# Optimization experiments

Hardware: AMD Instinct MI355X
Metric: run time of the kernel (lower is better)

The kernel has to match this reference:

```python
import jax, jax.numpy as jnp
import numpy as np
from jax import lax


def setup_inputs() -> dict:
    key = jax.random.key(0)
    k1, k2 = jax.random.split(key)
    L, B, D = 1024, 16, 1024
    x = jax.random.normal(k1, (L, B, D), dtype=jnp.float32)
    # weight maps n_in -> n_out*k with k=3 (n_in == n_out); small scale for stability
    weight = jax.random.normal(k2, (D, 3 * D), dtype=jnp.float32) * 0.05
    bias = jnp.zeros((2 * D,), dtype=jnp.float32)
    c0 = jnp.zeros((B, D), dtype=jnp.float32)
    return {"x": x, "weight": weight, "bias": bias, "c0": c0}


def reference(x, weight, bias, c0):
    # SRUCell forward, k == 3 (n_in == n_out), unidirectional, tanh activation,
    # no dropout masks (mask_h == NULL -> mask = 1).
    L, B, D = x.shape
    u = (x.reshape(L * B, D) @ weight).reshape(L, B, D, 3)
    b1 = bias[:D]
    b2 = bias[D:]
    u0 = u[..., 0]                                   # [L, B, D]
    g1 = jax.nn.sigmoid(u[..., 1] + b1)              # forget gate
    g2 = jax.nn.sigmoid(u[..., 2] + b2)              # reset/highway gate

    def step(c, inp):
        u0_t, g1_t, g2_t, x_t = inp
        c_new = (c - u0_t) * g1_t + u0_t             # c = c'*g1 + u0*(1-g1)
        h_t = (jnp.tanh(c_new) - x_t) * g2_t + x_t   # h = act(c)*g2 + x*(1-g2)
        return c_new, h_t

    c_last, h = lax.scan(step, c0, (u0, g1, g2, x))
    return h, c_last
```

## Files before the change

### kernel.cpp

```cpp
#include <hip/hip_runtime.h>

#define L_DIM 1024
#define B_DIM 16
#define D_DIM 1024
#define K_DIM 1024
#define N_DIM 3072
#define M_DIM (L_DIM * B_DIM)
#define CHAINS 16384
#define CHUNK 64
#define NCHUNK 16

typedef float f32x4 __attribute__((ext_vector_type(4)));
typedef __bf16 bf16x8 __attribute__((ext_vector_type(8)));
typedef unsigned short u16;
typedef unsigned int u32;

__device__ __forceinline__ u16 f2bf(float f) {
  u32 u = __float_as_uint(f);
  u = u + 0x7FFFu + ((u >> 16) & 1u);
  return (u16)(u >> 16);
}
__device__ __forceinline__ float bf2f(u16 v) {
  return __uint_as_float(((u32)v) << 16);
}
__device__ __forceinline__ float fexp(float v) {
  return __builtin_amdgcn_exp2f(v * 1.4426950408889634f);
}
__device__ __forceinline__ float sigm(float z) {
  return __builtin_amdgcn_rcpf(1.0f + fexp(-z));
}
__device__ __forceinline__ float ftanh(float v) {
  return 1.0f - 2.0f * __builtin_amdgcn_rcpf(1.0f + fexp(2.0f * v));
}

__global__ __launch_bounds__(256) void cvt_x_kernel(const float4* __restrict__ in,
                                                    ushort4* __restrict__ out, int n4) {
  int i = blockIdx.x * 256 + threadIdx.x;
  if (i < n4) {
    float4 v = in[i];
    ushort4 o;
    o.x = f2bf(v.x); o.y = f2bf(v.y); o.z = f2bf(v.z); o.w = f2bf(v.w);
    out[i] = o;
  }
}

__global__ __launch_bounds__(256) void cvt_w_kernel(const float* __restrict__ W,
                                                    u16* __restrict__ Wt) {
  __shared__ float tile[64][65];
  int c0 = blockIdx.x * 64;
  int r0 = blockIdx.y * 64;
  int tx = threadIdx.x & 63;
  int ty = threadIdx.x >> 6;
#pragma unroll
  for (int i = 0; i < 16; ++i) {
    int row = i * 4 + ty;
    tile[row][tx] = W[(size_t)(r0 + row) * N_DIM + c0 + tx];
  }
  __syncthreads();
#pragma unroll
  for (int i = 0; i < 16; ++i) {
    int crow = i * 4 + ty;
    int c = c0 + crow;
    int nprime = (c % 3) * D_DIM + (c / 3);
    Wt[(size_t)nprime * K_DIM + r0 + tx] = f2bf(tile[tx][crow]);
  }
}

__global__ __launch_bounds__(256) void gemm_kernel(const u16* __restrict__ A,
                                                   const u16* __restrict__ Bt,
                                                   u16* __restrict__ U) {
  __shared__ u16 lA[128 * 32];
  __shared__ u16 lB[128 * 32];
  const int tid = threadIdx.x;
  const int wave = tid >> 6;
  const int lane = tid & 63;
  const int wm = wave >> 1, wn = wave & 1;
  const int quad = lane >> 4, l16 = lane & 15;
  const int m0 = blockIdx.y * 128;
  const int n0 = blockIdx.x * 128;

  f32x4 acc[4][4] = {};

  const u16* gA = A + (size_t)(m0 + (tid >> 2)) * K_DIM + (tid & 3) * 8;
  const u16* gB = Bt + (size_t)(n0 + (tid >> 2)) * K_DIM + (tid & 3) * 8;
  u16* sA0 = lA + wave * 512;
  u16* sA1 = lA + 2048 + wave * 512;
  u16* sB0 = lB + wave * 512;
  u16* sB1 = lB + 2048 + wave * 512;

  const u16* rA = lA + (wm * 64 + l16) * 32 + quad * 8;
  const u16* rB = lB + (wn * 64 + l16) * 32 + quad * 8;

  for (int k0 = 0; k0 < K_DIM; k0 += 32) {
    __syncthreads();
    __builtin_amdgcn_global_load_lds((const __attribute__((address_space(1))) void*)(gA + k0),
                                     (__attribute__((address_space(3))) void*)sA0, 16, 0, 0);
    __builtin_amdgcn_global_load_lds((const __attribute__((address_space(1))) void*)(gA + (size_t)64 * K_DIM + k0),
                                     (__attribute__((address_space(3))) void*)sA1, 16, 0, 0);
    __builtin_amdgcn_global_load_lds((const __attribute__((address_space(1))) void*)(gB + k0),
                                     (__attribute__((address_space(3))) void*)sB0, 16, 0, 0);
    __builtin_amdgcn_global_load_lds((const __attribute__((address_space(1))) void*)(gB + (size_t)64 * K_DIM + k0),
                                     (__attribute__((address_space(3))) void*)sB1, 16, 0, 0);
    __syncthreads();

    bf16x8 af[4], bfr[4];
#pragma unroll
    for (int mt = 0; mt < 4; ++mt) af[mt] = *(const bf16x8*)(rA + mt * 16 * 32);
#pragma unroll
    for (int nt = 0; nt < 4; ++nt) bfr[nt] = *(const bf16x8*)(rB + nt * 16 * 32);
#pragma unroll
    for (int mt = 0; mt < 4; ++mt)
#pragma unroll
      for (int nt = 0; nt < 4; ++nt)
        acc[mt][nt] = __builtin_amdgcn_mfma_f32_16x16x32_bf16(af[mt], bfr[nt], acc[mt][nt], 0, 0, 0);
  }

#pragma unroll
  for (int mt = 0; mt < 4; ++mt) {
#pragma unroll
    for (int nt = 0; nt < 4; ++nt) {
      int col = n0 + wn * 64 + nt * 16 + l16;
      int rbase = m0 + wm * 64 + mt * 16 + quad * 4;
#pragma unroll
      for (int r = 0; r < 4; ++r) {
        U[(size_t)(rbase + r) * N_DIM + col] = f2bf(acc[mt][nt][r]);
      }
    }
  }
}


__global__ __launch_bounds__(256) void sru_phase1(const u16* __restrict__ U,
                                                  const float* __restrict__ bias,
                                                  float* __restrict__ Aarr,
                                                  float* __restrict__ Barr) {
  int tid = blockIdx.x * 256 + threadIdx.x;
  int chain = tid & (CHAINS - 1);
  int j = tid >> 14;
  int d = chain & (D_DIM - 1);
  int b = chain >> 10;
  float bb1 = bias[d];
  const u16* p = U + (size_t)(j * CHUNK * B_DIM + b) * N_DIM + d;
  float A = 1.0f, Bv = 0.0f;
#pragma unroll 4
  for (int s = 0; s < CHUNK; ++s) {
    float u0 = bf2f(p[0]);
    float g1 = sigm(bf2f(p[D_DIM]) + bb1);
    Bv = (Bv - u0) * g1 + u0;
    A *= g1;
    p += (size_t)B_DIM * N_DIM;
  }
  Aarr[tid] = A;
  Barr[tid] = Bv;
}

__global__ __launch_bounds__(256) void sru_phase2(const float* __restrict__ Aarr,
                                                  const float* __restrict__ Barr,
                                                  const float* __restrict__ c0,
                                                  float* __restrict__ Cin,
                                                  float* __restrict__ clast) {
  int chain = blockIdx.x * 256 + threadIdx.x;
  float As[NCHUNK], Bs[NCHUNK];
#pragma unroll
  for (int j = 0; j < NCHUNK; ++j) {
    As[j] = Aarr[j * CHAINS + chain];
    Bs[j] = Barr[j * CHAINS + chain];
  }
  float c = c0[chain];
#pragma unroll
  for (int j = 0; j < NCHUNK; ++j) {
    Cin[j * CHAINS + chain] = c;
    c = As[j] * c + Bs[j];
  }
  clast[chain] = c;
}

__global__ __launch_bounds__(256) void sru_phase3(const u16* __restrict__ U,
                                                  const float* __restrict__ x,
                                                  const float* __restrict__ bias,
                                                  const float* __restrict__ Cin,
                                                  float* __restrict__ h) {
  int tid = blockIdx.x * 256 + threadIdx.x;
  int chain = tid & (CHAINS - 1);
  int j = tid >> 14;
  int d = chain & (D_DIM - 1);
  int b = chain >> 10;
  float bb1 = bias[d];
  float bb2 = bias[D_DIM + d];
  float c = Cin[tid];
  size_t m0 = (size_t)(j * CHUNK * B_DIM + b);
  const u16* p = U + m0 * N_DIM + d;
  const float* xp = x + m0 * D_DIM + d;
  float* hp = h + m0 * D_DIM + d;
#pragma unroll 4
  for (int s = 0; s < CHUNK; ++s) {
    float u0 = bf2f(p[0]);
    float g1 = sigm(bf2f(p[D_DIM]) + bb1);
    float g2 = sigm(bf2f(p[2 * D_DIM]) + bb2);
    c = (c - u0) * g1 + u0;
    float xv = *xp;
    *hp = (ftanh(c) - xv) * g2 + xv;
    p += (size_t)B_DIM * N_DIM;
    xp += B_DIM * D_DIM;
    hp += B_DIM * D_DIM;
  }
}

extern "C" void kernel_launch(void* const* d_in, const int* in_sizes, int n_in,
                              void* d_out, int out_size, void* d_ws, size_t ws_size,
                              hipStream_t stream) {
  const float* x = (const float*)d_in[0];
  const float* W = (const float*)d_in[1];
  const float* bias = (const float*)d_in[2];
  const float* c0 = (const float*)d_in[3];
  float* out = (float*)d_out;

  char* ws = (char*)d_ws;
  u16* xb = (u16*)ws;
  u16* wt = (u16*)(ws + 33554432);
  u16* U = (u16*)(ws + 33554432 + 6291456);
  float* Aarr = (float*)ws;
  float* Barr = (float*)(ws + 1048576);
  float* Cin  = (float*)(ws + 2097152);

  cvt_x_kernel<<<16384, 256, 0, stream>>>((const float4*)x, (ushort4*)xb, M_DIM * K_DIM / 4);
  cvt_w_kernel<<<dim3(48, 16), 256, 0, stream>>>(W, wt);
  gemm_kernel<<<dim3(N_DIM / 128, M_DIM / 128), 256, 0, stream>>>(xb, wt, U);
  sru_phase1<<<CHAINS * NCHUNK / 256, 256, 0, stream>>>(U, bias, Aarr, Barr);
  sru_phase2<<<CHAINS / 256, 256, 0, stream>>>(Aarr, Barr, c0, Cin, out + (size_t)M_DIM * D_DIM);
  sru_phase3<<<CHAINS * NCHUNK / 256, 256, 0, stream>>>(U, x, bias, Cin, out);
}
```

Before: 299.9 us.

## Stage GEMM output through LDS and vectorize scan phases eight channels per thread

The GEMM epilogue now writes bf16 results into a padded LDS tile and then stores 16-byte rows to global memory, replacing scattered 2-byte stores. The scan phases 1 and 3 now process eight adjacent channels per thread with 16-byte loads of U, x and h. The chunk count is doubled (32 chunks of 32 steps) so enough threads remain for parallelism, and the Aarr/Barr/Cin workspace offsets grow to match. Phase 2 now reads Aarr/Barr inside the loop instead of preloading them into register arrays, and the added chunks lengthen its serial chain.

```diff
diff --git a/kernel.cpp b/kernel.cpp
--- a/kernel.cpp
+++ b/kernel.cpp
@@ -7,13 +7,14 @@
 #define N_DIM 3072
 #define M_DIM (L_DIM * B_DIM)
 #define CHAINS 16384
-#define CHUNK 64
-#define NCHUNK 16
+#define CHUNK 32
+#define NCHUNK 32
 
 typedef float f32x4 __attribute__((ext_vector_type(4)));
 typedef __bf16 bf16x8 __attribute__((ext_vector_type(8)));
 typedef unsigned short u16;
 typedef unsigned int u32;
+typedef u16 u16x8 __attribute__((ext_vector_type(8)));
 
 __device__ __forceinline__ u16 f2bf(float f) {
   u32 u = __float_as_uint(f);
@@ -69,8 +70,9 @@
 __global__ __launch_bounds__(256) void gemm_kernel(const u16* __restrict__ A,
                                                    const u16* __restrict__ Bt,
                                                    u16* __restrict__ U) {
-  __shared__ u16 lA[128 * 32];
-  __shared__ u16 lB[128 * 32];
+  __shared__ __align__(16) char smem[128 * 132 * 2];
+  u16* lA = (u16*)smem;
+  u16* lB = (u16*)(smem + 8192);
   const int tid = threadIdx.x;
   const int wave = tid >> 6;
   const int lane = tid & 63;
@@ -115,17 +117,30 @@
         acc[mt][nt] = __builtin_amdgcn_mfma_f32_16x16x32_bf16(af[mt], bfr[nt], acc[mt][nt], 0, 0, 0);
   }
 
+  __syncthreads();
+  u16* lC = (u16*)smem;
 #pragma unroll
   for (int mt = 0; mt < 4; ++mt) {
 #pragma unroll
     for (int nt = 0; nt < 4; ++nt) {
-      int col = n0 + wn * 64 + nt * 16 + l16;
-      int rbase = m0 + wm * 64 + mt * 16 + quad * 4;
-#pragma unroll
-      for (int r = 0; r < 4; ++r) {
-        U[(size_t)(rbase + r) * N_DIM + col] = f2bf(acc[mt][nt][r]);
-      }
+      int row = wm * 64 + mt * 16 + quad * 4;
+      int col = wn * 64 + nt * 16 + l16;
+#pragma unroll
+      for (int r = 0; r < 4; ++r)
+        lC[(row + r) * 132 + col] = f2bf(acc[mt][nt][r]);
     }
+  }
+  __syncthreads();
+  int g = tid & 15;
+  int r0w = tid >> 4;
+#pragma unroll
+  for (int it = 0; it < 8; ++it) {
+    int row = r0w + it * 16;
+    const u16* src = lC + row * 132 + g * 8;
+    uint2 lo = *(const uint2*)src;
+    uint2 hi = *(const uint2*)(src + 4);
+    uint4 v = make_uint4(lo.x, lo.y, hi.x, hi.y);
+    *(uint4*)(U + (size_t)(m0 + row) * N_DIM + n0 + g * 8) = v;
   }
 }
 
@@ -135,23 +150,37 @@
                                                   float* __restrict__ Aarr,
                                                   float* __restrict__ Barr) {
   int tid = blockIdx.x * 256 + threadIdx.x;
-  int chain = tid & (CHAINS - 1);
-  int j = tid >> 14;
-  int d = chain & (D_DIM - 1);
-  int b = chain >> 10;
-  float bb1 = bias[d];
-  const u16* p = U + (size_t)(j * CHUNK * B_DIM + b) * N_DIM + d;
-  float A = 1.0f, Bv = 0.0f;
+  int j = tid >> 11;
+  int b = (tid >> 7) & 15;
+  int dg = tid & 127;
+  int d0 = dg * 8;
+  int chain0 = b * D_DIM + d0;
+  float bb1[8];
+#pragma unroll
+  for (int i = 0; i < 8; ++i) bb1[i] = bias[d0 + i];
+  const u16* p = U + (size_t)(j * CHUNK * B_DIM + b) * N_DIM + d0;
+  float A[8], Bv[8];
+#pragma unroll
+  for (int i = 0; i < 8; ++i) { A[i] = 1.0f; Bv[i] = 0.0f; }
 #pragma unroll 4
   for (int s = 0; s < CHUNK; ++s) {
-    float u0 = bf2f(p[0]);
-    float g1 = sigm(bf2f(p[D_DIM]) + bb1);
-    Bv = (Bv - u0) * g1 + u0;
-    A *= g1;
+    u16x8 u0v = *(const u16x8*)p;
+    u16x8 g1v = *(const u16x8*)(p + D_DIM);
+#pragma unroll
+    for (int i = 0; i < 8; ++i) {
+      float u0 = bf2f(u0v[i]);
+      float g1 = sigm(bf2f(g1v[i]) + bb1[i]);
+      Bv[i] = (Bv[i] - u0) * g1 + u0;
+      A[i] *= g1;
+    }
     p += (size_t)B_DIM * N_DIM;
   }
-  Aarr[tid] = A;
-  Barr[tid] = Bv;
+  float* Ap = Aarr + (size_t)j * CHAINS + chain0;
+  float* Bp = Barr + (size_t)j * CHAINS + chain0;
+  *(float4*)Ap = make_float4(A[0], A[1], A[2], A[3]);
+  *(float4*)(Ap + 4) = make_float4(A[4], A[5], A[6], A[7]);
+  *(float4*)Bp = make_float4(Bv[0], Bv[1], Bv[2], Bv[3]);
+  *(float4*)(Bp + 4) = make_float4(Bv[4], Bv[5], Bv[6], Bv[7]);
 }
 
 __global__ __launch_bounds__(256) void sru_phase2(const float* __restrict__ Aarr,
@@ -160,17 +189,11 @@
                                                   float* __restrict__ Cin,
                                                   float* __restrict__ clast) {
   int chain = blockIdx.x * 256 + threadIdx.x;
-  float As[NCHUNK], Bs[NCHUNK];
-#pragma unroll
-  for (int j = 0; j < NCHUNK; ++j) {
-    As[j] = Aarr[j * CHAINS + chain];
-    Bs[j] = Barr[j * CHAINS + chain];
-  }
   float c = c0[chain];
 #pragma unroll
   for (int j = 0; j < NCHUNK; ++j) {
     Cin[j * CHAINS + chain] = c;
-    c = As[j] * c + Bs[j];
+    c = Aarr[j * CHAINS + chain] * c + Barr[j * CHAINS + chain];
   }
   clast[chain] = c;
 }
@@ -181,25 +204,43 @@
                                                   const float* __restrict__ Cin,
                                                   float* __restrict__ h) {
   int tid = blockIdx.x * 256 + threadIdx.x;
-  int chain = tid & (CHAINS - 1);
-  int j = tid >> 14;
-  int d = chain & (D_DIM - 1);
-  int b = chain >> 10;
-  float bb1 = bias[d];
-  float bb2 = bias[D_DIM + d];
-  float c = Cin[tid];
+  int j = tid >> 11;
+  int b = (tid >> 7) & 15;
+  int dg = tid & 127;
+  int d0 = dg * 8;
+  int chain0 = b * D_DIM + d0;
+  float bb1[8], bb2[8], c[8];
+#pragma unroll
+  for (int i = 0; i < 8; ++i) {
+    bb1[i] = bias[d0 + i];
+    bb2[i] = bias[D_DIM + d0 + i];
+  }
+  const float* cin = Cin + (size_t)j * CHAINS + chain0;
+#pragma unroll
+  for (int i = 0; i < 8; ++i) c[i] = cin[i];
   size_t m0 = (size_t)(j * CHUNK * B_DIM + b);
-  const u16* p = U + m0 * N_DIM + d;
-  const float* xp = x + m0 * D_DIM + d;
-  float* hp = h + m0 * D_DIM + d;
-#pragma unroll 4
+  const u16* p = U + m0 * N_DIM + d0;
+  const float* xp = x + m0 * D_DIM + d0;
+  float* hp = h + m0 * D_DIM + d0;
+#pragma unroll 2
   for (int s = 0; s < CHUNK; ++s) {
-    float u0 = bf2f(p[0]);
-    float g1 = sigm(bf2f(p[D_DIM]) + bb1);
-    float g2 = sigm(bf2f(p[2 * D_DIM]) + bb2);
-    c = (c - u0) * g1 + u0;
-    float xv = *xp;
-    *hp = (ftanh(c) - xv) * g2 + xv;
+    u16x8 u0v = *(const u16x8*)p;
+    u16x8 g1v = *(const u16x8*)(p + D_DIM);
+    u16x8 g2v = *(const u16x8*)(p + 2 * D_DIM);
+    float4 x0 = *(const float4*)xp;
+    float4 x1 = *(const float4*)(xp + 4);
+    float xs[8] = {x0.x, x0.y, x0.z, x0.w, x1.x, x1.y, x1.z, x1.w};
+    float hs[8];
+#pragma unroll
+    for (int i = 0; i < 8; ++i) {
+      float u0 = bf2f(u0v[i]);
+      float g1 = sigm(bf2f(g1v[i]) + bb1[i]);
+      float g2 = sigm(bf2f(g2v[i]) + bb2[i]);
+      c[i] = (c[i] - u0) * g1 + u0;
+      hs[i] = (ftanh(c[i]) - xs[i]) * g2 + xs[i];
+    }
+    *(float4*)hp = make_float4(hs[0], hs[1], hs[2], hs[3]);
+    *(float4*)(hp + 4) = make_float4(hs[4], hs[5], hs[6], hs[7]);
     p += (size_t)B_DIM * N_DIM;
     xp += B_DIM * D_DIM;
     hp += B_DIM * D_DIM;
@@ -220,13 +261,13 @@
   u16* wt = (u16*)(ws + 33554432);
   u16* U = (u16*)(ws + 33554432 + 6291456);
   float* Aarr = (float*)ws;
-  float* Barr = (float*)(ws + 1048576);
-  float* Cin  = (float*)(ws + 2097152);
+  float* Barr = (float*)(ws + 2097152);
+  float* Cin  = (float*)(ws + 4194304);
 
   cvt_x_kernel<<<16384, 256, 0, stream>>>((const float4*)x, (ushort4*)xb, M_DIM * K_DIM / 4);
   cvt_w_kernel<<<dim3(48, 16), 256, 0, stream>>>(W, wt);
   gemm_kernel<<<dim3(N_DIM / 128, M_DIM / 128), 256, 0, stream>>>(xb, wt, U);
-  sru_phase1<<<CHAINS * NCHUNK / 256, 256, 0, stream>>>(U, bias, Aarr, Barr);
+  sru_phase1<<<CHAINS * NCHUNK / 8 / 256, 256, 0, stream>>>(U, bias, Aarr, Barr);
   sru_phase2<<<CHAINS / 256, 256, 0, stream>>>(Aarr, Barr, c0, Cin, out + (size_t)M_DIM * D_DIM);
-  sru_phase3<<<CHAINS * NCHUNK / 256, 256, 0, stream>>>(U, x, bias, Cin, out);
-}
+  sru_phase3<<<CHAINS * NCHUNK / 8 / 256, 256, 0, stream>>>(U, x, bias, Cin, out);
+}
```

Result: slower. 316.4 us (+5.5%).
